# Kernel optimization log

Measured on AMD Instinct MI355X. Metric: run time of the kernel, lower is better.

The kernel has to match this reference:

```python
import jax, jax.numpy as jnp
import numpy as np

EPS = 1e-06


def setup_inputs() -> dict:
    key = jax.random.key(0)
    k1, k2 = jax.random.split(key)
    x = jax.random.normal(k1, (16, 64, 256, 256), dtype=jnp.float32)
    gamma = jax.random.normal(k2, (1,), dtype=jnp.float32)
    return {"x": x, "gamma": gamma}


def reference(x, gamma):
    B, C, H, W = x.shape
    N = H * W
    v = x.reshape(B, C, N)                      # Q = K = V = flattened x
    # l2_norm: normalize across channel dim (dim=-2) per spatial position
    inv_norm = 1.0 / (jnp.linalg.norm(v, axis=1) + 1e-06)   # [B, N]
    qn = v * inv_norm[:, None, :]               # [B, C, N], Q and K normalized identically
    q_sum = jnp.sum(qn, axis=1)                 # [B, N] (sum over channels)
    # tailor_sum: 1 / (N + K^T-summed-Q + eps) -> [B, C]
    tailor = 1.0 / (N + jnp.einsum('bcn,bn->bc', qn, q_sum) + EPS)
    value_sum = jnp.sum(v, axis=1)[:, None, :]  # [B, 1, N], broadcasts over C
    matrix = jnp.einsum('bcn,bmn->bcm', v, qn)  # V @ K^T : [B, C, C]
    matrix_sum = value_sum + jnp.einsum('bcm,bmn->bcn', matrix, qn)  # [B, C, N]
    weight_value = matrix_sum * tailor[:, :, None]
    return x + gamma * weight_value.reshape(B, C, H, W)
```

## Files before the change

kernel.cpp:

```cpp
#include <hip/hip_runtime.h>
#include <stdint.h>

#define BATCH 16
#define CDIM 64
#define NDIM 65536
#define EPSV 1e-6f

typedef __attribute__((ext_vector_type(8))) short bf16x8;
typedef __attribute__((ext_vector_type(4))) short bf16x4;
typedef __attribute__((ext_vector_type(4))) float f32x4;

static __device__ __forceinline__ uint32_t f2bf(float f) {
    uint32_t u = __builtin_bit_cast(uint32_t, f);
    return (u + 0x7fffu + ((u >> 16) & 1u)) >> 16;
}
static __device__ __forceinline__ float bf2f(uint32_t h) {
    uint32_t u = h << 16;
    return __builtin_bit_cast(float, u);
}

#define T1 256
#define P1 264
#define CHUNKS 4
#define NTILE1 64

__global__ __launch_bounds__(256, 4)
void gram_kernel(const float* __restrict__ x, float* __restrict__ pmat,
                 float* __restrict__ pt) {
    __shared__ __align__(16) short ldsU[CDIM][P1];
    __shared__ __align__(16) float ldsG[T1];
    __shared__ float red[4][CDIM];

    const int tid = threadIdx.x;
    const int b = blockIdx.x >> 6;
    const int tileIdx = blockIdx.x & 63;
    const int w = tid >> 6;
    const int lane = tid & 63;
    const int cq = lane >> 4;
    const int cr = lane & 15;

    f32x4 acc0 = {0.f, 0.f, 0.f, 0.f};
    f32x4 acc1 = acc0, acc2 = acc0, acc3 = acc0;
    float tpart = 0.f;

    const float* xbase = x + (size_t)b * CDIM * NDIM;

    for (int chunk = 0; chunk < CHUNKS; ++chunk) {
        const int n0 = tileIdx * (T1 * CHUNKS) + chunk * T1;
        const float* xb = xbase + n0 + tid;
        float ss = 0.f, cs = 0.f;
#pragma unroll 8
        for (int c = 0; c < CDIM; ++c) {
            float v = xb[(size_t)c * NDIM];
            ss += v * v;
            cs += v;
            ldsU[c][tid] = (short)f2bf(v);
        }
        const float inv = 1.f / (sqrtf(ss) + EPSV);
        const float sq = sqrtf(inv);
        ldsG[tid] = inv * sq * cs;
#pragma unroll 8
        for (int c = 0; c < CDIM; ++c) {
            uint32_t h = (uint16_t)ldsU[c][tid];
            ldsU[c][tid] = (short)f2bf(bf2f(h) * sq);
        }
        __syncthreads();
#pragma unroll
        for (int ks = 0; ks < 8; ++ks) {
            const int k0 = ks * 32 + cq * 8;
            bf16x8 afrag = *(const bf16x8*)&ldsU[w * 16 + cr][k0];
            bf16x8 b0 = *(const bf16x8*)&ldsU[cr][k0];
            bf16x8 b1 = *(const bf16x8*)&ldsU[16 + cr][k0];
            bf16x8 b2 = *(const bf16x8*)&ldsU[32 + cr][k0];
            bf16x8 b3 = *(const bf16x8*)&ldsU[48 + cr][k0];
            acc0 = __builtin_amdgcn_mfma_f32_16x16x32_bf16(afrag, b0, acc0, 0, 0, 0);
            acc1 = __builtin_amdgcn_mfma_f32_16x16x32_bf16(afrag, b1, acc1, 0, 0, 0);
            acc2 = __builtin_amdgcn_mfma_f32_16x16x32_bf16(afrag, b2, acc2, 0, 0, 0);
            acc3 = __builtin_amdgcn_mfma_f32_16x16x32_bf16(afrag, b3, acc3, 0, 0, 0);
        }
#pragma unroll
        for (int i = 0; i < 8; ++i) {
            const int nb = w * 64 + i * 8;
            bf16x8 uf = *(const bf16x8*)&ldsU[lane][nb];
            f32x4 g0 = *(const f32x4*)&ldsG[nb];
            f32x4 g1 = *(const f32x4*)&ldsG[nb + 4];
#pragma unroll
            for (int j = 0; j < 4; ++j) {
                tpart += bf2f((uint32_t)(uint16_t)uf[j]) * g0[j];
                tpart += bf2f((uint32_t)(uint16_t)uf[j + 4]) * g1[j];
            }
        }
        __syncthreads();
    }
    red[w][lane] = tpart;
    __syncthreads();
    if (tid < CDIM) {
        pt[(size_t)blockIdx.x * CDIM + tid] =
            red[0][tid] + red[1][tid] + red[2][tid] + red[3][tid];
    }
    float* pm = pmat + (size_t)blockIdx.x * CDIM * CDIM;
    const f32x4 accs[4] = {acc0, acc1, acc2, acc3};
#pragma unroll
    for (int mt = 0; mt < 4; ++mt) {
#pragma unroll
        for (int r = 0; r < 4; ++r) {
            const int row = w * 16 + cq * 4 + r;
            const int col = mt * 16 + cr;
            pm[row * CDIM + col] = accs[mt][r];
        }
    }
}

__global__ __launch_bounds__(256, 4)
void reduce_kernel(const float* __restrict__ pmat, const float* __restrict__ pt,
                   float* __restrict__ mat, float* __restrict__ tl) {
    const int blk = blockIdx.x;
    const int tid = threadIdx.x;
    if (blk < 256) {
        const int b = blk >> 4;
        const int o = (blk & 15) * 256 + tid;
        float s = 0.f;
#pragma unroll 8
        for (int t = 0; t < NTILE1; ++t)
            s += pmat[((size_t)(b * NTILE1 + t)) * (CDIM * CDIM) + o];
        mat[b * CDIM * CDIM + o] = s;
    } else {
        const int idx = (blk - 256) * 256 + tid;
        const int b = idx >> 6;
        const int c = idx & 63;
        float s = 0.f;
#pragma unroll 8
        for (int t = 0; t < NTILE1; ++t)
            s += pt[(size_t)(b * NTILE1 + t) * CDIM + c];
        tl[idx] = 1.f / ((float)NDIM + s + EPSV);
    }
}

#define T2 256
#define P2 68
#define PM 72

__global__ __launch_bounds__(256, 3)
void out_kernel(const float* __restrict__ x, const float* __restrict__ mat,
                const float* __restrict__ tl, const float* __restrict__ gamma,
                float* __restrict__ out) {
    __shared__ __align__(16) short ldsV[T2][P2];
    __shared__ __align__(16) short ldsM[CDIM][PM];
    __shared__ float ldsCS[T2];
    __shared__ float ldsIN[T2];
    __shared__ float ldsTL[CDIM];

    const int tid = threadIdx.x;
    const int bid = (int)(gridDim.x - 1 - blockIdx.x);
    const int b = bid >> 8;
    const int n0 = (bid & 255) * T2;
    const int w = tid >> 6;
    const int lane = tid & 63;
    const int cq = lane >> 4;
    const int cr = lane & 15;

    const float* mb = mat + (size_t)b * CDIM * CDIM;
#pragma unroll
    for (int i = 0; i < 16; ++i) {
        const int idx = tid + i * 256;
        ldsM[idx >> 6][idx & 63] = (short)f2bf(mb[idx]);
    }
    if (tid < CDIM) ldsTL[tid] = tl[b * CDIM + tid];

    const float* xb = x + (size_t)b * CDIM * NDIM + n0 + tid;
    float ss = 0.f, cs = 0.f;
#pragma unroll 8
    for (int cp = 0; cp < 32; ++cp) {
        float v0 = xb[(size_t)(2 * cp) * NDIM];
        float v1 = xb[(size_t)(2 * cp + 1) * NDIM];
        ss += v0 * v0 + v1 * v1;
        cs += v0 + v1;
        *(uint32_t*)&ldsV[tid][2 * cp] = f2bf(v0) | (f2bf(v1) << 16);
    }
    ldsIN[tid] = 1.f / (sqrtf(ss) + EPSV);
    ldsCS[tid] = cs;
    __syncthreads();

    bf16x8 afrag[4][2];
#pragma unroll
    for (int ct = 0; ct < 4; ++ct)
#pragma unroll
        for (int ks = 0; ks < 2; ++ks)
            afrag[ct][ks] = *(const bf16x8*)&ldsM[ct * 16 + cr][ks * 32 + cq * 8];

    f32x4 acc[4][4];
#pragma unroll
    for (int p = 0; p < 4; ++p)
#pragma unroll
        for (int ct = 0; ct < 4; ++ct)
            acc[p][ct] = (f32x4){0.f, 0.f, 0.f, 0.f};

#pragma unroll
    for (int p = 0; p < 4; ++p) {
        const int n = (w * 4 + p) * 16 + cr;
#pragma unroll
        for (int ks = 0; ks < 2; ++ks) {
            const int k0 = ks * 32 + cq * 8;
            bf16x4 lo = *(const bf16x4*)&ldsV[n][k0];
            bf16x4 hi = *(const bf16x4*)&ldsV[n][k0 + 4];
            bf16x8 bfrag = __builtin_shufflevector(lo, hi, 0, 1, 2, 3, 4, 5, 6, 7);
#pragma unroll
            for (int ct = 0; ct < 4; ++ct)
                acc[p][ct] = __builtin_amdgcn_mfma_f32_16x16x32_bf16(
                    afrag[ct][ks], bfrag, acc[p][ct], 0, 0, 0);
        }
    }

    const float g = gamma[0];
    float* ob = out + (size_t)b * CDIM * NDIM + n0;
#pragma unroll
    for (int p = 0; p < 4; ++p) {
        const int n = (w * 4 + p) * 16 + cr;
        const float csn = ldsCS[n];
        const float invn = ldsIN[n];
#pragma unroll
        for (int ct = 0; ct < 4; ++ct) {
            const int c0 = ct * 16 + cq * 4;
            bf16x4 xv4 = *(const bf16x4*)&ldsV[n][c0];
#pragma unroll
            for (int r = 0; r < 4; ++r) {
                const int c = c0 + r;
                ob[(size_t)c * NDIM + n] =
                    bf2f((uint32_t)(uint16_t)xv4[r]) +
                    g * ldsTL[c] * (csn + invn * acc[p][ct][r]);
            }
        }
    }
}

extern "C" void kernel_launch(void* const* d_in, const int* in_sizes, int n_in,
                              void* d_out, int out_size, void* d_ws, size_t ws_size,
                              hipStream_t stream) {
    const float* x = (const float*)d_in[0];
    const float* gamma = (const float*)d_in[1];
    float* out = (float*)d_out;
    float* pmat = (float*)d_ws;
    float* pt = pmat + (size_t)1024 * CDIM * CDIM;
    float* mat = pt + (size_t)1024 * CDIM;
    float* tl = mat + BATCH * CDIM * CDIM;
    hipLaunchKernelGGL(gram_kernel, dim3(BATCH * NTILE1), dim3(256), 0, stream,
                       x, pmat, pt);
    hipLaunchKernelGGL(reduce_kernel, dim3(260), dim3(256), 0, stream,
                       pmat, pt, mat, tl);
    hipLaunchKernelGGL(out_kernel, dim3(BATCH * 256), dim3(256), 0, stream,
                       x, mat, tl, gamma, out);
}
```

Measured before the change: 555.5 us.

## Vectorize gram loads, compute tailor sum via MFMA, load matrix fragments directly

In the gram kernel, each wave now loads 16 channels with float4 vector loads instead of one thread walking all 64 channels per column. The per-column sum of squares and channel sum are combined across waves through LDS, packed as bf16. The tailor reduction moves from a scalar dot-product loop onto extra MFMA instructions that use a bf16 g-vector fragment. In the output kernel, the matrix fragments are read straight from global memory into registers, dropping the LDS staging, and accumulators are kept per p-iteration to cut register use, with launch bounds raised to 4. The bf16 packing of partial sums and of g adds rounding error to the normalization and tailor terms.

```diff
diff --git a/kernel.cpp b/kernel.cpp
--- a/kernel.cpp
+++ b/kernel.cpp
@@ -9,15 +9,26 @@
 typedef __attribute__((ext_vector_type(8))) short bf16x8;
 typedef __attribute__((ext_vector_type(4))) short bf16x4;
 typedef __attribute__((ext_vector_type(4))) float f32x4;
-
-static __device__ __forceinline__ uint32_t f2bf(float f) {
+typedef __attribute__((ext_vector_type(4))) uint32_t u32x4;
+typedef __attribute__((ext_vector_type(2))) uint32_t u32x2;
+
+static __device__ __forceinline__ uint32_t rne_u(float f) {
     uint32_t u = __builtin_bit_cast(uint32_t, f);
-    return (u + 0x7fffu + ((u >> 16) & 1u)) >> 16;
+    return u + 0x7fffu + ((u >> 16) & 1u);
+}
+static __device__ __forceinline__ uint32_t pk_rne(float a, float b) {
+    return __builtin_amdgcn_perm(rne_u(a), rne_u(b), 0x03020706u);
+}
+static __device__ __forceinline__ float bf_lo(uint32_t u) {
+    return __builtin_bit_cast(float, u << 16);
+}
+static __device__ __forceinline__ float bf_hi(uint32_t u) {
+    return __builtin_bit_cast(float, u & 0xffff0000u);
 }
 static __device__ __forceinline__ float bf2f(uint32_t h) {
-    uint32_t u = h << 16;
-    return __builtin_bit_cast(float, u);
-}
+    return __builtin_bit_cast(float, h << 16);
+}
+static __device__ __forceinline__ uint32_t f2bf(float f) { return rne_u(f) >> 16; }
 
 #define T1 256
 #define P1 264
@@ -28,47 +39,84 @@
 void gram_kernel(const float* __restrict__ x, float* __restrict__ pmat,
                  float* __restrict__ pt) {
     __shared__ __align__(16) short ldsU[CDIM][P1];
-    __shared__ __align__(16) float ldsG[T1];
-    __shared__ float red[4][CDIM];
+    __shared__ __align__(16) short ldsGbf[T1];
+    __shared__ __align__(16) uint32_t red[4][T1];
 
     const int tid = threadIdx.x;
     const int b = blockIdx.x >> 6;
     const int tileIdx = blockIdx.x & 63;
     const int w = tid >> 6;
-    const int lane = tid & 63;
-    const int cq = lane >> 4;
-    const int cr = lane & 15;
+    const int l = tid & 63;
+    const int cq = l >> 4;
+    const int cr = l & 15;
 
     f32x4 acc0 = {0.f, 0.f, 0.f, 0.f};
     f32x4 acc1 = acc0, acc2 = acc0, acc3 = acc0;
-    float tpart = 0.f;
-
-    const float* xbase = x + (size_t)b * CDIM * NDIM;
+    f32x4 at0 = acc0, at1 = acc0, at2 = acc0, at3 = acc0;
+
+    const float* xbase = x + (size_t)b * CDIM * NDIM + (size_t)(w * 16) * NDIM;
 
     for (int chunk = 0; chunk < CHUNKS; ++chunk) {
         const int n0 = tileIdx * (T1 * CHUNKS) + chunk * T1;
-        const float* xb = xbase + n0 + tid;
-        float ss = 0.f, cs = 0.f;
-#pragma unroll 8
-        for (int c = 0; c < CDIM; ++c) {
-            float v = xb[(size_t)c * NDIM];
-            ss += v * v;
-            cs += v;
-            ldsU[c][tid] = (short)f2bf(v);
-        }
-        const float inv = 1.f / (sqrtf(ss) + EPSV);
-        const float sq = sqrtf(inv);
-        ldsG[tid] = inv * sq * cs;
-#pragma unroll 8
-        for (int c = 0; c < CDIM; ++c) {
-            uint32_t h = (uint16_t)ldsU[c][tid];
-            ldsU[c][tid] = (short)f2bf(bf2f(h) * sq);
+        const float* xb = xbase + n0 + 4 * l;
+        f32x4 ssp = {0.f, 0.f, 0.f, 0.f};
+        f32x4 csp = ssp;
+        u32x2 raw[16];
+#pragma unroll
+        for (int i = 0; i < 16; ++i) {
+            f32x4 v = *(const f32x4*)(xb + (size_t)i * NDIM);
+            ssp += v * v;
+            csp += v;
+            raw[i].x = pk_rne(v.x, v.y);
+            raw[i].y = pk_rne(v.z, v.w);
+        }
+        u32x4 pk;
+#pragma unroll
+        for (int j = 0; j < 4; ++j) pk[j] = pk_rne(ssp[j], csp[j]);
+        *(u32x4*)&red[w][4 * l] = pk;
+        __syncthreads();
+        f32x4 ss = {0.f, 0.f, 0.f, 0.f};
+        f32x4 cs = ss;
+#pragma unroll
+        for (int ww = 0; ww < 4; ++ww) {
+            u32x4 q = *(const u32x4*)&red[ww][4 * l];
+#pragma unroll
+            for (int j = 0; j < 4; ++j) {
+                ss[j] += bf_lo(q[j]);
+                cs[j] += bf_hi(q[j]);
+            }
+        }
+        f32x4 sq, gv;
+#pragma unroll
+        for (int j = 0; j < 4; ++j) {
+            float inv = 1.f / (sqrtf(ss[j]) + EPSV);
+            float s = sqrtf(inv);
+            sq[j] = s;
+            gv[j] = inv * s * cs[j];
+        }
+        if (w == 0) {
+            u32x2 gw;
+            gw.x = pk_rne(gv[0], gv[1]);
+            gw.y = pk_rne(gv[2], gv[3]);
+            *(u32x2*)&ldsGbf[4 * l] = gw;
+        }
+#pragma unroll
+        for (int i = 0; i < 16; ++i) {
+            float f0 = bf_lo(raw[i].x) * sq[0];
+            float f1 = bf_hi(raw[i].x) * sq[1];
+            float f2 = bf_lo(raw[i].y) * sq[2];
+            float f3 = bf_hi(raw[i].y) * sq[3];
+            u32x2 uw;
+            uw.x = pk_rne(f0, f1);
+            uw.y = pk_rne(f2, f3);
+            *(u32x2*)&ldsU[w * 16 + i][4 * l] = uw;
         }
         __syncthreads();
 #pragma unroll
         for (int ks = 0; ks < 8; ++ks) {
             const int k0 = ks * 32 + cq * 8;
             bf16x8 afrag = *(const bf16x8*)&ldsU[w * 16 + cr][k0];
+            bf16x8 gfrag = *(const bf16x8*)&ldsGbf[k0];
             bf16x8 b0 = *(const bf16x8*)&ldsU[cr][k0];
             bf16x8 b1 = *(const bf16x8*)&ldsU[16 + cr][k0];
             bf16x8 b2 = *(const bf16x8*)&ldsU[32 + cr][k0];
@@ -77,26 +125,19 @@
             acc1 = __builtin_amdgcn_mfma_f32_16x16x32_bf16(afrag, b1, acc1, 0, 0, 0);
             acc2 = __builtin_amdgcn_mfma_f32_16x16x32_bf16(afrag, b2, acc2, 0, 0, 0);
             acc3 = __builtin_amdgcn_mfma_f32_16x16x32_bf16(afrag, b3, acc3, 0, 0, 0);
-        }
-#pragma unroll
-        for (int i = 0; i < 8; ++i) {
-            const int nb = w * 64 + i * 8;
-            bf16x8 uf = *(const bf16x8*)&ldsU[lane][nb];
-            f32x4 g0 = *(const f32x4*)&ldsG[nb];
-            f32x4 g1 = *(const f32x4*)&ldsG[nb + 4];
-#pragma unroll
-            for (int j = 0; j < 4; ++j) {
-                tpart += bf2f((uint32_t)(uint16_t)uf[j]) * g0[j];
-                tpart += bf2f((uint32_t)(uint16_t)uf[j + 4]) * g1[j];
-            }
+            at0 = __builtin_amdgcn_mfma_f32_16x16x32_bf16(gfrag, b0, at0, 0, 0, 0);
+            at1 = __builtin_amdgcn_mfma_f32_16x16x32_bf16(gfrag, b1, at1, 0, 0, 0);
+            at2 = __builtin_amdgcn_mfma_f32_16x16x32_bf16(gfrag, b2, at2, 0, 0, 0);
+            at3 = __builtin_amdgcn_mfma_f32_16x16x32_bf16(gfrag, b3, at3, 0, 0, 0);
         }
         __syncthreads();
     }
-    red[w][lane] = tpart;
-    __syncthreads();
-    if (tid < CDIM) {
-        pt[(size_t)blockIdx.x * CDIM + tid] =
-            red[0][tid] + red[1][tid] + red[2][tid] + red[3][tid];
+    if (tid < 16) {
+        float* ptb = pt + (size_t)blockIdx.x * CDIM;
+        ptb[tid] = at0[0];
+        ptb[16 + tid] = at1[0];
+        ptb[32 + tid] = at2[0];
+        ptb[48 + tid] = at3[0];
     }
     float* pm = pmat + (size_t)blockIdx.x * CDIM * CDIM;
     const f32x4 accs[4] = {acc0, acc1, acc2, acc3};
@@ -138,14 +179,12 @@
 
 #define T2 256
 #define P2 68
-#define PM 72
-
-__global__ __launch_bounds__(256, 3)
+
+__global__ __launch_bounds__(256, 4)
 void out_kernel(const float* __restrict__ x, const float* __restrict__ mat,
                 const float* __restrict__ tl, const float* __restrict__ gamma,
                 float* __restrict__ out) {
     __shared__ __align__(16) short ldsV[T2][P2];
-    __shared__ __align__(16) short ldsM[CDIM][PM];
     __shared__ float ldsCS[T2];
     __shared__ float ldsIN[T2];
     __shared__ float ldsTL[CDIM];
@@ -159,13 +198,24 @@
     const int cq = lane >> 4;
     const int cr = lane & 15;
 
+    if (tid < CDIM) ldsTL[tid] = tl[b * CDIM + tid];
+
     const float* mb = mat + (size_t)b * CDIM * CDIM;
-#pragma unroll
-    for (int i = 0; i < 16; ++i) {
-        const int idx = tid + i * 256;
-        ldsM[idx >> 6][idx & 63] = (short)f2bf(mb[idx]);
-    }
-    if (tid < CDIM) ldsTL[tid] = tl[b * CDIM + tid];
+    bf16x8 afrag[4][2];
+#pragma unroll
+    for (int ct = 0; ct < 4; ++ct)
+#pragma unroll
+        for (int ks = 0; ks < 2; ++ks) {
+            const float* ap = mb + (ct * 16 + cr) * CDIM + ks * 32 + cq * 8;
+            f32x4 m0 = *(const f32x4*)ap;
+            f32x4 m1 = *(const f32x4*)(ap + 4);
+            u32x4 pkv;
+            pkv.x = pk_rne(m0.x, m0.y);
+            pkv.y = pk_rne(m0.z, m0.w);
+            pkv.z = pk_rne(m1.x, m1.y);
+            pkv.w = pk_rne(m1.z, m1.w);
+            afrag[ct][ks] = __builtin_bit_cast(bf16x8, pkv);
+        }
 
     const float* xb = x + (size_t)b * CDIM * NDIM + n0 + tid;
     float ss = 0.f, cs = 0.f;
@@ -175,47 +225,36 @@
         float v1 = xb[(size_t)(2 * cp + 1) * NDIM];
         ss += v0 * v0 + v1 * v1;
         cs += v0 + v1;
-        *(uint32_t*)&ldsV[tid][2 * cp] = f2bf(v0) | (f2bf(v1) << 16);
+        *(uint32_t*)&ldsV[tid][2 * cp] = pk_rne(v0, v1);
     }
     ldsIN[tid] = 1.f / (sqrtf(ss) + EPSV);
     ldsCS[tid] = cs;
     __syncthreads();
 
-    bf16x8 afrag[4][2];
-#pragma unroll
-    for (int ct = 0; ct < 4; ++ct)
-#pragma unroll
-        for (int ks = 0; ks < 2; ++ks)
-            afrag[ct][ks] = *(const bf16x8*)&ldsM[ct * 16 + cr][ks * 32 + cq * 8];
-
-    f32x4 acc[4][4];
-#pragma unroll
-    for (int p = 0; p < 4; ++p)
-#pragma unroll
-        for (int ct = 0; ct < 4; ++ct)
-            acc[p][ct] = (f32x4){0.f, 0.f, 0.f, 0.f};
+    const float g = gamma[0];
+    float* ob = out + (size_t)b * CDIM * NDIM + n0;
 
 #pragma unroll
     for (int p = 0; p < 4; ++p) {
         const int n = (w * 4 + p) * 16 + cr;
+        bf16x8 bfr[2];
 #pragma unroll
         for (int ks = 0; ks < 2; ++ks) {
             const int k0 = ks * 32 + cq * 8;
             bf16x4 lo = *(const bf16x4*)&ldsV[n][k0];
             bf16x4 hi = *(const bf16x4*)&ldsV[n][k0 + 4];
-            bf16x8 bfrag = __builtin_shufflevector(lo, hi, 0, 1, 2, 3, 4, 5, 6, 7);
+            bfr[ks] = __builtin_shufflevector(lo, hi, 0, 1, 2, 3, 4, 5, 6, 7);
+        }
+        f32x4 acc[4];
+#pragma unroll
+        for (int ct = 0; ct < 4; ++ct) acc[ct] = (f32x4){0.f, 0.f, 0.f, 0.f};
+#pragma unroll
+        for (int ks = 0; ks < 2; ++ks)
 #pragma unroll
             for (int ct = 0; ct < 4; ++ct)
-                acc[p][ct] = __builtin_amdgcn_mfma_f32_16x16x32_bf16(
-                    afrag[ct][ks], bfrag, acc[p][ct], 0, 0, 0);
-        }
-    }
-
-    const float g = gamma[0];
-    float* ob = out + (size_t)b * CDIM * NDIM + n0;
-#pragma unroll
-    for (int p = 0; p < 4; ++p) {
-        const int n = (w * 4 + p) * 16 + cr;
+                acc[ct] = __builtin_amdgcn_mfma_f32_16x16x32_bf16(
+                    afrag[ct][ks], bfr[ks], acc[ct], 0, 0, 0);
+
         const float csn = ldsCS[n];
         const float invn = ldsIN[n];
 #pragma unroll
@@ -227,7 +266,7 @@
                 const int c = c0 + r;
                 ob[(size_t)c * NDIM + n] =
                     bf2f((uint32_t)(uint16_t)xv4[r]) +
-                    g * ldsTL[c] * (csn + invn * acc[p][ct][r]);
+                    g * ldsTL[c] * (csn + invn * acc[ct][r]);
             }
         }
     }
```

New measurement: 593.9 us. 1.07x slower.
